# Kernel optimization log

Hardware: AMD Instinct MI355X
Metric: run time of the kernel (lower is better)

Reference implementation:

```python
import jax, jax.numpy as jnp
import numpy as np

MAX_DIST = 8
GUIDANCE_WEIGHT = 0.4
EPS_MAG = 1e-6
EPS_COS = 1e-8
EPS_WSUM = 1e-8


def setup_inputs() -> dict:
    key = jax.random.key(0)
    k1, k2 = jax.random.split(key)
    embeddings = jax.random.normal(k1, (4, 2048, 1024), dtype=jnp.float32)
    guidance_trajectories = jax.random.normal(k2, (512, 1024), dtype=jnp.float32)
    return {"embeddings": embeddings, "guidance_trajectories": guidance_trajectories}


def reference(embeddings, guidance_trajectories):
    B, S, D = embeddings.shape
    W = min(MAX_DIST, S - 1)  # fixed max window size

    # consecutive-token trajectory vectors: diffs[t] = emb[t+1] - emb[t]
    diffs = embeddings[:, 1:, :] - embeddings[:, :-1, :]          # [B, S-1, D]

    # sliding windows of the last W diffs ending at pos-1
    pos = jnp.arange(S)[:, None]                                  # [S, 1]
    k = jnp.arange(W)[None, :]                                    # [1, W]
    idx = pos - W + k                                             # diff index per slot
    valid = (idx >= 0) & (pos >= 1)                               # [S, W]
    windows = diffs[:, jnp.clip(idx, 0, S - 2), :]                # [B, S, W, D]

    # torch.linspace(0.1, 1.0, w) weights, per-position window size w = min(pos, W);
    # valid entries occupy the last w slots of the W-wide window.
    w = jnp.minimum(pos, W)                                       # [S, 1]
    j = k - (W - w)                                               # local index within window
    lin = jnp.where(w > 1, 0.1 + 0.9 * j / jnp.maximum(w - 1, 1), 0.1)
    pos_weights = jnp.where(valid, lin, 0.0).astype(embeddings.dtype)  # [S, W]

    # normalize trajectory vectors, zero where magnitude <= 1e-6
    mag = jnp.linalg.norm(windows, axis=-1, keepdims=True)        # [B, S, W, 1]
    is_valid_mag = mag > EPS_MAG
    normed = jnp.where(is_valid_mag, windows / jnp.where(is_valid_mag, mag, 1.0), 0.0)

    mag_weights = jnp.tanh(mag * 2.0)                             # [B, S, W, 1]
    combined = pos_weights[None, :, :, None] * mag_weights        # [B, S, W, 1]

    # guidance influence: softmax over cosine similarity to guidance bank
    g_norm = jnp.linalg.norm(guidance_trajectories, axis=-1)      # [G]
    a_norm = jnp.linalg.norm(normed, axis=-1)                     # [B, S, W]
    dots = jnp.einsum('bswd,gd->bswg', normed, guidance_trajectories)
    sims = dots / (jnp.maximum(a_norm, EPS_COS)[..., None] * jnp.maximum(g_norm, EPS_COS))
    g_weights = jax.nn.softmax(sims * 2.0, axis=-1)               # [B, S, W, G]
    influence = jnp.einsum('bswg,gd->bswd', g_weights, guidance_trajectories)
    blended = (1.0 - GUIDANCE_WEIGHT) * normed + GUIDANCE_WEIGHT * influence

    weight_sum = jnp.maximum(combined.sum(axis=2), EPS_WSUM)      # [B, S, 1]
    trajectories = (blended * combined).sum(axis=2) / weight_sum  # [B, S, D]
    return trajectories
```

## Files before the change

### kernel.cpp

```cpp
#include <hip/hip_runtime.h>
#include <math.h>

#define B_ 4
#define S_ 2048
#define D_ 1024
#define G_ 512
#define MTO 32
#define NR 48
#define DHST 1032
#define WST 520
#define IPST 1032
#define D8ST 1040
#define VST 520

typedef __attribute__((ext_vector_type(8))) short short8;
typedef __attribute__((ext_vector_type(4))) short s16x4;
typedef __attribute__((ext_vector_type(4))) float f32x4;
typedef __attribute__((ext_vector_type(4))) int i32x4;

#define WSOFF_RG2 0u
#define WSOFF_BP1 4096u
#define WSOFF_BP2 528384u

__device__ inline short to_bf16(float f) {
    union { float f; unsigned u; } v; v.f = f;
    unsigned r = v.u + 0x7fffu + ((v.u >> 16) & 1u);
    return (short)(r >> 16);
}
__device__ inline float fb(unsigned short h) {
    union { unsigned u; float f; } v;
    v.u = ((unsigned)h) << 16;
    return v.f;
}
__device__ inline float fbs(short h) { return fb((unsigned short)h); }
__device__ inline f32x4 MF(short8 a, short8 b, f32x4 c) {
    return __builtin_amdgcn_mfma_f32_16x16x32_bf16(a, b, c, 0, 0, 0);
}
__device__ inline i32x4 MFI(i32x4 a, i32x4 b, i32x4 c) {
    return __builtin_amdgcn_mfma_i32_16x16x64_i8(a, b, c, 0, 0, 0);
}
__device__ inline unsigned pk4(float x, float y, float z, float w, float qs) {
    int a = (int)rintf(x * qs), b = (int)rintf(y * qs);
    int c = (int)rintf(z * qs), d = (int)rintf(w * qs);
    return (unsigned)(a & 255) | ((unsigned)(b & 255) << 8) |
           ((unsigned)(c & 255) << 16) | ((unsigned)(d & 255) << 24);
}

#define RAWBAR() do {                                            \
    __builtin_amdgcn_sched_barrier(0);                           \
    asm volatile("s_waitcnt lgkmcnt(0)" ::: "memory");           \
    __builtin_amdgcn_s_barrier();                                \
    __builtin_amdgcn_sched_barrier(0);                           \
} while (0)

__global__ __launch_bounds__(256) void prep_kernel(const float* __restrict__ guid,
                                                   float* __restrict__ rg2q,
                                                   i32x4* __restrict__ Bp1q,
                                                   short8* __restrict__ Bp2) {
    int bid = blockIdx.x, tid = threadIdx.x;
    if (bid < 128) {
        int wave = tid >> 6, lane = tid & 63;
        int g = bid * 4 + wave;
        const float4* g4 = (const float4*)(guid + (size_t)g * D_);
        float4 v[4]; float ss = 0.f, mx = 0.f;
#pragma unroll
        for (int c = 0; c < 4; ++c) {
            float4 t = g4[lane * 4 + c]; v[c] = t;
            ss += t.x * t.x + t.y * t.y + t.z * t.z + t.w * t.w;
            mx = fmaxf(mx, fmaxf(fmaxf(fabsf(t.x), fabsf(t.y)),
                                 fmaxf(fabsf(t.z), fabsf(t.w))));
        }
#pragma unroll
        for (int m = 32; m >= 1; m >>= 1) {
            ss += __shfl_xor(ss, m, 64);
            mx = fmaxf(mx, __shfl_xor(mx, m, 64));
        }
        if (lane == 0) rg2q[g] = 2.f * (mx / 127.f) / fmaxf(sqrtf(ss), 1e-8f);
        float qs = 127.f / fmaxf(mx, 1e-20f);
        i32x4 o;
#pragma unroll
        for (int c = 0; c < 4; ++c) o[c] = (int)pk4(v[c].x, v[c].y, v[c].z, v[c].w, qs);
        Bp1q[(size_t)lane * G_ + g] = o;
    } else {
        int gg = bid - 128;
#pragma unroll
        for (int dd = 0; dd < 4; ++dd) {
            int d = tid + 256 * dd;
            short8 v;
#pragma unroll
            for (int j = 0; j < 8; ++j) v[j] = to_bf16(guid[(size_t)(gg * 8 + j) * D_ + d]);
            Bp2[(size_t)gg * D_ + d] = v;
        }
    }
}

#define G1S(ksv, q)  {                                                            \
    const char* abp = D8 + (ksv) * 64 + quad * 16;                                \
    i32x4 a0 = *(const i32x4*)(abp + (size_t)l15 * D8ST);                         \
    i32x4 a1 = *(const i32x4*)(abp + (size_t)(16 + l15) * D8ST);                  \
    i32x4 a2 = *(const i32x4*)(abp + (size_t)(32 + l15) * D8ST);                  \
    acc1[0][0] = MFI(a0, q[0], acc1[0][0]); acc1[0][1] = MFI(a0, q[1], acc1[0][1]); \
    acc1[1][0] = MFI(a1, q[0], acc1[1][0]); acc1[1][1] = MFI(a1, q[1], acc1[1][1]); \
    acc1[2][0] = MFI(a2, q[0], acc1[2][0]); acc1[2][1] = MFI(a2, q[1], acc1[2][1]); }

__global__ __launch_bounds__(1024, 4) void fused_kernel(const float* __restrict__ emb,
                                                        const i32x4* __restrict__ Bp1q,
                                                        const short8* __restrict__ Bp2,
                                                        const float* __restrict__ rg2q,
                                                        float* __restrict__ out) {
    __shared__ __align__(16) char RA[80512];
    __shared__ __align__(16) char RB[49920];
    __shared__ float rg2s[G_];
    __shared__ float pred[NR][16];
    __shared__ float magS[NR], rmvqS[NR], mrS[NR];
    __shared__ float rwsS[MTO];

    short* DH = (short*)RA;
    short* WD = (short*)RA;
    short* IP = (short*)RA;
    char*  D8 = RB;
    short* V  = (short*)RB;

    const int tid = threadIdx.x;
    const int wave = tid >> 6, lane = tid & 63;
    const int l15 = lane & 15, quad = lane >> 4;
    const int bid = blockIdx.x;
    const int b = bid >> 6;
    const int s0 = (bid & 63) << 5;
    const bool edge = (s0 == 0);

    if (tid < G_) rg2s[tid] = rg2q[tid];

    for (int ii = 0; ii < 3; ++ii) {
        int rr = wave + 16 * ii;
        int t = s0 - 8 + rr;
        bool val = (t >= 0) && (rr < 39);
        float ss = 0.f, mx = 0.f;
        float4 dv[4];
        if (val) {
            const float4* p = (const float4*)(emb + ((size_t)b * S_ + t) * D_);
#pragma unroll
            for (int j = 0; j < 4; ++j) {
                float4 x0 = p[lane + 64 * j];
                float4 x1 = p[lane + 64 * j + 256];
                float4 d = make_float4(x1.x - x0.x, x1.y - x0.y, x1.z - x0.z, x1.w - x0.w);
                dv[j] = d;
                ss += d.x * d.x + d.y * d.y + d.z * d.z + d.w * d.w;
                mx = fmaxf(mx, fmaxf(fmaxf(fabsf(d.x), fabsf(d.y)),
                                     fmaxf(fabsf(d.z), fabsf(d.w))));
            }
        } else {
#pragma unroll
            for (int j = 0; j < 4; ++j) dv[j] = make_float4(0.f, 0.f, 0.f, 0.f);
        }
#pragma unroll
        for (int m = 32; m >= 1; m >>= 1) {
            ss += __shfl_xor(ss, m, 64);
            mx = fmaxf(mx, __shfl_xor(mx, m, 64));
        }
        float mag = sqrtf(ss);
        if (lane == 0) {
            bool ok = val && (mag > 1e-6f);
            float tw = tanhf(2.f * mag);
            magS[rr]  = val ? tw : 0.f;
            rmvqS[rr] = ok ? mx / (127.f * mag) : 0.f;
            mrS[rr]   = ok ? 0.6f * tw / mag : 0.f;
        }
        float qs = 127.f / fmaxf(mx, 1e-20f);
#pragma unroll
        for (int j = 0; j < 4; ++j) {
            if (rr < 39) {
                s16x4 h;
                h[0] = to_bf16(dv[j].x); h[1] = to_bf16(dv[j].y);
                h[2] = to_bf16(dv[j].z); h[3] = to_bf16(dv[j].w);
                *(s16x4*)&DH[(size_t)rr * DHST + 4 * lane + 256 * j] = h;
            }
            *(unsigned*)&D8[(size_t)rr * D8ST + 4 * lane + 256 * j] =
                val ? pk4(dv[j].x, dv[j].y, dv[j].z, dv[j].w, qs) : 0u;
        }
    }
    RAWBAR();

    if (tid < MTO) {
        int w = edge ? ((tid < 8) ? tid : 8) : 8;
        float rw = (w > 1) ? 0.9f / (float)(w - 1) : 0.f;
        float s = 0.f;
#pragma unroll
        for (int a = 1; a <= 8; ++a) {
            float lin = (a <= w) ? ((w > 1) ? (0.1f + rw * (float)(w - a)) : 0.1f) : 0.f;
            s += lin * magS[tid + 8 - a];
        }
        rwsS[tid] = 1.0f / fmaxf(s, 1e-8f);
    }

    i32x4 acc1[3][2];
#pragma unroll
    for (int mt = 0; mt < 3; ++mt)
#pragma unroll
        for (int nt = 0; nt < 2; ++nt) acc1[mt][nt] = (i32x4)0;
    {
        const i32x4* PB = Bp1q + (size_t)quad * G_ + wave * 32 + l15;
        i32x4 q0[2], q1[2], q2[2], q3[2];
        q0[0] = PB[0];        q0[1] = PB[16];
        q1[0] = PB[2048];     q1[1] = PB[2048 + 16];
        q2[0] = PB[4096];     q2[1] = PB[4096 + 16];
        q3[0] = PB[6144];     q3[1] = PB[6144 + 16];
#pragma unroll
        for (int k4 = 0; k4 < 16; k4 += 4) {
            G1S(k4 + 0, q0); if (k4 < 12) { q0[0] = PB[(size_t)(k4 + 4) * 2048]; q0[1] = PB[(size_t)(k4 + 4) * 2048 + 16]; }
            G1S(k4 + 1, q1); if (k4 < 12) { q1[0] = PB[(size_t)(k4 + 5) * 2048]; q1[1] = PB[(size_t)(k4 + 5) * 2048 + 16]; }
            G1S(k4 + 2, q2); if (k4 < 12) { q2[0] = PB[(size_t)(k4 + 6) * 2048]; q2[1] = PB[(size_t)(k4 + 6) * 2048 + 16]; }
            G1S(k4 + 3, q3); if (k4 < 12) { q3[0] = PB[(size_t)(k4 + 7) * 2048]; q3[1] = PB[(size_t)(k4 + 7) * 2048 + 16]; }
        }
    }

    float np_[MTO];
    {
        float pr[8];
#pragma unroll
        for (int r = 0; r < 8; ++r) pr[r] = mrS[r] * fbs(DH[(size_t)r * DHST + tid]);
        if (!edge) {
#pragma unroll
            for (int i = 0; i < MTO; ++i) {
                float s = 0.f;
#pragma unroll
                for (int a = 1; a <= 8; ++a)
                    s += (0.1f + (0.9f / 7.f) * (float)(8 - a)) * pr[(i + 8 - a) & 7];
                np_[i] = s;
                if (i < 31) pr[i & 7] = mrS[i + 8] * fbs(DH[(size_t)(i + 8) * DHST + tid]);
            }
        } else {
#pragma unroll
            for (int i = 0; i < MTO; ++i) {
                int w = (i < 8) ? i : 8;
                float rw = (w > 1) ? 0.9f / (float)(w - 1) : 0.f;
                float s = 0.f;
#pragma unroll
                for (int a = 1; a <= 8; ++a) {
                    float lin = (a <= w) ? ((w > 1) ? (0.1f + rw * (float)(w - a)) : 0.1f) : 0.f;
                    s += lin * pr[(i + 8 - a) & 7];
                }
                np_[i] = s;
                if (i < 31) pr[i & 7] = mrS[i + 8] * fbs(DH[(size_t)(i + 8) * DHST + tid]);
            }
        }
    }

    float psum[3][4];
    {
        float rmv[3][4];
#pragma unroll
        for (int mt = 0; mt < 3; ++mt)
#pragma unroll
            for (int r2 = 0; r2 < 4; ++r2) {
                rmv[mt][r2] = rmvqS[mt * 16 + quad * 4 + r2];
                psum[mt][r2] = 0.f;
            }
#pragma unroll
        for (int mt = 0; mt < 3; ++mt)
#pragma unroll
            for (int nt = 0; nt < 2; ++nt) {
                float rgv = rg2s[wave * 32 + nt * 16 + l15];
#pragma unroll
                for (int r2 = 0; r2 < 4; ++r2) {
                    float e = __expf((float)acc1[mt][nt][r2] * rgv * rmv[mt][r2]);
                    acc1[mt][nt][r2] = __float_as_int(e);
                    psum[mt][r2] += e;
                }
            }
#pragma unroll
        for (int m = 8; m >= 1; m >>= 1)
#pragma unroll
            for (int mt = 0; mt < 3; ++mt)
#pragma unroll
                for (int r2 = 0; r2 < 4; ++r2)
                    psum[mt][r2] += __shfl_xor(psum[mt][r2], m, 16);
    }
    RAWBAR();

#pragma unroll
    for (int mt = 0; mt < 3; ++mt)
#pragma unroll
        for (int nt = 0; nt < 2; ++nt)
#pragma unroll
            for (int r2 = 0; r2 < 4; ++r2)
                WD[(size_t)(mt * 16 + quad * 4 + r2) * WST + wave * 32 + nt * 16 + l15] =
                    to_bf16(__int_as_float(acc1[mt][nt][r2]));
    if (l15 == 0) {
#pragma unroll
        for (int mt = 0; mt < 3; ++mt)
#pragma unroll
            for (int r2 = 0; r2 < 4; ++r2)
                pred[mt * 16 + quad * 4 + r2][wave] = psum[mt][r2];
    }
    RAWBAR();

    {
        float sums[9];
#pragma unroll
        for (int r = 0; r < 9; ++r) {
            int rr = 2 * wave + r;
            float s = 0.f;
#pragma unroll
            for (int w2 = 0; w2 < 16; ++w2) s += pred[rr][w2];
            sums[r] = s;
        }
#pragma unroll
        for (int ii = 0; ii < 2; ++ii) {
            int i = wave * 2 + ii;
            int w = edge ? ((i < 8) ? i : 8) : 8;
            float rw = (w > 1) ? 0.9f / (float)(w - 1) : 0.f;
            float c[8];
#pragma unroll
            for (int a = 1; a <= 8; ++a) {
                int rr = i + 8 - a;
                float lin = (a <= w) ? ((w > 1) ? (0.1f + rw * (float)(w - a)) : 0.1f) : 0.f;
                c[a - 1] = lin * 0.4f * magS[rr] / sums[rr - 2 * wave];
            }
            float v[8];
#pragma unroll
            for (int j = 0; j < 8; ++j) v[j] = 0.f;
#pragma unroll
            for (int a = 1; a <= 8; ++a) {
                short8 e = *(const short8*)&WD[(size_t)(i + 8 - a) * WST + lane * 8];
#pragma unroll
                for (int j = 0; j < 8; ++j) v[j] += c[a - 1] * fbs(e[j]);
            }
            short8 vo;
#pragma unroll
            for (int j = 0; j < 8; ++j) vo[j] = to_bf16(v[j]);
            *(short8*)&V[(size_t)i * VST + lane * 8] = vo;
        }
    }
    RAWBAR();

#pragma unroll
    for (int half = 0; half < 2; ++half) {
        f32x4 acc2[2][2];
#pragma unroll
        for (int mt = 0; mt < 2; ++mt)
#pragma unroll
            for (int nt = 0; nt < 2; ++nt) acc2[mt][nt] = (f32x4)0.f;
        const short8* Bb2 = Bp2 + (size_t)quad * D_ + wave * 64 + half * 32 + l15;
        short8 bc0 = Bb2[0], bc1 = Bb2[16], bn0, bn1;
#pragma unroll
        for (int ks = 0; ks < 16; ++ks) {
            if (ks < 15) {
                const short8* Bx = Bb2 + (size_t)(ks + 1) * 4 * D_;
                bn0 = Bx[0]; bn1 = Bx[16];
            }
            short8 a0 = *(const short8*)&V[(size_t)l15 * VST + ks * 32 + quad * 8];
            short8 a1 = *(const short8*)&V[(size_t)(16 + l15) * VST + ks * 32 + quad * 8];
            acc2[0][0] = MF(a0, bc0, acc2[0][0]); acc2[0][1] = MF(a0, bc1, acc2[0][1]);
            acc2[1][0] = MF(a1, bc0, acc2[1][0]); acc2[1][1] = MF(a1, bc1, acc2[1][1]);
            bc0 = bn0; bc1 = bn1;
        }
#pragma unroll
        for (int mt = 0; mt < 2; ++mt)
#pragma unroll
            for (int ntl = 0; ntl < 2; ++ntl) {
                int d2 = wave * 64 + half * 32 + ntl * 16 + l15;
#pragma unroll
                for (int r2 = 0; r2 < 4; ++r2)
                    IP[(size_t)(mt * 16 + quad * 4 + r2) * IPST + d2] =
                        to_bf16(acc2[mt][ntl][r2]);
            }
    }
    RAWBAR();

    {
        float* ob = out + ((size_t)b * S_ + s0) * D_ + tid;
#pragma unroll
        for (int i = 0; i < MTO; ++i) {
            float ip = fbs(IP[(size_t)i * IPST + tid]);
            ob[(size_t)i * D_] = (np_[i] + ip) * rwsS[i];
        }
    }
}

extern "C" void kernel_launch(void* const* d_in, const int* in_sizes, int n_in,
                              void* d_out, int out_size, void* d_ws, size_t ws_size,
                              hipStream_t stream) {
    const float* emb  = (const float*)d_in[0];
    const float* guid = (const float*)d_in[1];
    float* out = (float*)d_out;
    char* ws = (char*)d_ws;

    float* rg2q = (float*)(ws + WSOFF_RG2);
    i32x4* Bp1q = (i32x4*)(ws + WSOFF_BP1);
    short8* Bp2 = (short8*)(ws + WSOFF_BP2);

    prep_kernel<<<192, 256, 0, stream>>>(guid, rg2q, Bp1q, Bp2);
    fused_kernel<<<256, 1024, 0, stream>>>(emb, Bp1q, Bp2, rg2q, out);
}
```

Measured before the change: 141.9 us.

## Swizzle block order, precompute per-row softmax coefficients once, add barriers

Block indices are remapped so consecutive hardware blocks map to different batch/sequence tiles, which changes the L2/cache access pattern across the grid. Per-row magnitude terms (mrS, and a new cvS holding 0.4*tanh(mag)/softmax-sum) are now computed once by a few threads instead of redundantly inside every wave. Each wave previously summed 9 rows × 16 partials itself. The cost is two extra block barriers, and tanh is now stored for invalid rows, which relies on zeroed data there.

Measured after the change: 115.1 us. 18.9% less time.

```diff
diff --git a/kernel.cpp b/kernel.cpp
--- a/kernel.cpp
+++ b/kernel.cpp
@@ -112,7 +112,7 @@
     __shared__ __align__(16) char RB[49920];
     __shared__ float rg2s[G_];
     __shared__ float pred[NR][16];
-    __shared__ float magS[NR], rmvqS[NR], mrS[NR];
+    __shared__ float magS[NR], rmagS[NR], rmvqS[NR], mrS[NR], cvS[NR];
     __shared__ float rwsS[MTO];
 
     short* DH = (short*)RA;
@@ -124,20 +124,22 @@
     const int tid = threadIdx.x;
     const int wave = tid >> 6, lane = tid & 63;
     const int l15 = lane & 15, quad = lane >> 4;
-    const int bid = blockIdx.x;
+    const int bid0 = blockIdx.x;
+    const int bid = ((bid0 & 7) << 5) | (bid0 >> 3);
     const int b = bid >> 6;
     const int s0 = (bid & 63) << 5;
     const bool edge = (s0 == 0);
 
     if (tid < G_) rg2s[tid] = rg2q[tid];
 
+#pragma unroll
     for (int ii = 0; ii < 3; ++ii) {
         int rr = wave + 16 * ii;
         int t = s0 - 8 + rr;
-        bool val = (t >= 0) && (rr < 39);
+        bool valid = (t >= 0) && (rr < 39);
         float ss = 0.f, mx = 0.f;
         float4 dv[4];
-        if (val) {
+        if (valid) {
             const float4* p = (const float4*)(emb + ((size_t)b * S_ + t) * D_);
 #pragma unroll
             for (int j = 0; j < 4; ++j) {
@@ -160,11 +162,10 @@
         }
         float mag = sqrtf(ss);
         if (lane == 0) {
-            bool ok = val && (mag > 1e-6f);
-            float tw = tanhf(2.f * mag);
-            magS[rr]  = val ? tw : 0.f;
-            rmvqS[rr] = ok ? mx / (127.f * mag) : 0.f;
-            mrS[rr]   = ok ? 0.6f * tw / mag : 0.f;
+            float rmag = (mag > 1e-6f) ? (1.0f / mag) : 0.0f;
+            magS[rr]  = tanhf(2.0f * mag);
+            rmagS[rr] = rmag;
+            rmvqS[rr] = rmag * (mx / 127.f);
         }
         float qs = 127.f / fmaxf(mx, 1e-20f);
 #pragma unroll
@@ -176,11 +177,12 @@
                 *(s16x4*)&DH[(size_t)rr * DHST + 4 * lane + 256 * j] = h;
             }
             *(unsigned*)&D8[(size_t)rr * D8ST + 4 * lane + 256 * j] =
-                val ? pk4(dv[j].x, dv[j].y, dv[j].z, dv[j].w, qs) : 0u;
-        }
-    }
-    RAWBAR();
-
+                valid ? pk4(dv[j].x, dv[j].y, dv[j].z, dv[j].w, qs) : 0u;
+        }
+    }
+    RAWBAR();
+
+    if (tid < NR) mrS[tid] = 0.6f * magS[tid] * rmagS[tid];
     if (tid < MTO) {
         int w = edge ? ((tid < 8) ? tid : 8) : 8;
         float rw = (w > 1) ? 0.9f / (float)(w - 1) : 0.f;
@@ -213,6 +215,7 @@
             G1S(k4 + 3, q3); if (k4 < 12) { q3[0] = PB[(size_t)(k4 + 7) * 2048]; q3[1] = PB[(size_t)(k4 + 7) * 2048 + 16]; }
         }
     }
+    RAWBAR();
 
     float np_[MTO];
     {
@@ -247,15 +250,16 @@
     }
 
     float psum[3][4];
+#pragma unroll
+    for (int mt = 0; mt < 3; ++mt)
+#pragma unroll
+        for (int r2 = 0; r2 < 4; ++r2) psum[mt][r2] = 0.f;
     {
         float rmv[3][4];
 #pragma unroll
         for (int mt = 0; mt < 3; ++mt)
 #pragma unroll
-            for (int r2 = 0; r2 < 4; ++r2) {
-                rmv[mt][r2] = rmvqS[mt * 16 + quad * 4 + r2];
-                psum[mt][r2] = 0.f;
-            }
+            for (int r2 = 0; r2 < 4; ++r2) rmv[mt][r2] = rmvqS[mt * 16 + quad * 4 + r2];
 #pragma unroll
         for (int mt = 0; mt < 3; ++mt)
 #pragma unroll
@@ -294,43 +298,38 @@
                 pred[mt * 16 + quad * 4 + r2][wave] = psum[mt][r2];
     }
     RAWBAR();
-
-    {
-        float sums[9];
-#pragma unroll
-        for (int r = 0; r < 9; ++r) {
-            int rr = 2 * wave + r;
-            float s = 0.f;
-#pragma unroll
-            for (int w2 = 0; w2 < 16; ++w2) s += pred[rr][w2];
-            sums[r] = s;
-        }
-#pragma unroll
-        for (int ii = 0; ii < 2; ++ii) {
-            int i = wave * 2 + ii;
-            int w = edge ? ((i < 8) ? i : 8) : 8;
-            float rw = (w > 1) ? 0.9f / (float)(w - 1) : 0.f;
-            float c[8];
-#pragma unroll
-            for (int a = 1; a <= 8; ++a) {
-                int rr = i + 8 - a;
-                float lin = (a <= w) ? ((w > 1) ? (0.1f + rw * (float)(w - a)) : 0.1f) : 0.f;
-                c[a - 1] = lin * 0.4f * magS[rr] / sums[rr - 2 * wave];
-            }
-            float v[8];
-#pragma unroll
-            for (int j = 0; j < 8; ++j) v[j] = 0.f;
-#pragma unroll
-            for (int a = 1; a <= 8; ++a) {
-                short8 e = *(const short8*)&WD[(size_t)(i + 8 - a) * WST + lane * 8];
-#pragma unroll
-                for (int j = 0; j < 8; ++j) v[j] += c[a - 1] * fbs(e[j]);
-            }
-            short8 vo;
-#pragma unroll
-            for (int j = 0; j < 8; ++j) vo[j] = to_bf16(v[j]);
-            *(short8*)&V[(size_t)i * VST + lane * 8] = vo;
-        }
+    if (tid < NR) {
+        float s = 0.f;
+#pragma unroll
+        for (int w2 = 0; w2 < 16; ++w2) s += pred[tid][w2];
+        cvS[tid] = 0.4f * magS[tid] / s;
+    }
+    RAWBAR();
+
+#pragma unroll
+    for (int ii = 0; ii < 2; ++ii) {
+        int i = wave * 2 + ii;
+        int w = edge ? ((i < 8) ? i : 8) : 8;
+        float rw = (w > 1) ? 0.9f / (float)(w - 1) : 0.f;
+        float c[8];
+#pragma unroll
+        for (int a = 1; a <= 8; ++a) {
+            float lin = (a <= w) ? ((w > 1) ? (0.1f + rw * (float)(w - a)) : 0.1f) : 0.f;
+            c[a - 1] = lin * cvS[i + 8 - a];
+        }
+        float v[8];
+#pragma unroll
+        for (int j = 0; j < 8; ++j) v[j] = 0.f;
+#pragma unroll
+        for (int a = 1; a <= 8; ++a) {
+            short8 e = *(const short8*)&WD[(size_t)(i + 8 - a) * WST + lane * 8];
+#pragma unroll
+            for (int j = 0; j < 8; ++j) v[j] += c[a - 1] * fbs(e[j]);
+        }
+        short8 vo;
+#pragma unroll
+        for (int j = 0; j < 8; ++j) vo[j] = to_bf16(v[j]);
+        *(short8*)&V[(size_t)i * VST + lane * 8] = vo;
     }
     RAWBAR();
 
```
